# Kernel tuning notes

Hardware: AMD Instinct MI355X
Metric: run time of the kernel (lower is better)

Reference implementation:

```python
import jax, jax.numpy as jnp
import numpy as np

T, B, D, H, L = 64, 512, 1536, 1024, 4
DISCOUNT = 0.997
LAM = 0.95


def setup_inputs() -> dict:
    key = jax.random.key(0)
    ks = jax.random.split(key, 3 + L + 1)
    inp = {
        'feat': jax.random.normal(ks[0], (T, B, D), dtype=jnp.float32),
        'reward': jax.random.normal(ks[1], (T - 1, B), dtype=jnp.float32),
        'cont': jnp.ones((T, B), dtype=jnp.float32),
    }
    scale = 0.02
    dims = [D] + [H] * L
    for i in range(L):
        inp[f'W{i}'] = jax.random.normal(ks[3 + i], (dims[i], dims[i + 1]), dtype=jnp.float32) * scale
        inp[f'b{i}'] = jnp.zeros((dims[i + 1],), dtype=jnp.float32)
    inp['Wo'] = jax.random.normal(ks[3 + L], (H,), dtype=jnp.float32) * scale
    inp['bo'] = jnp.zeros((), dtype=jnp.float32)
    return inp


def reference(feat, reward, cont, W0, b0, W1, b1, W2, b2, W3, b3, Wo, bo):
    # Value-net MLP (mean of critic dist): [T, B, D] -> [T, B]
    h = feat
    for W, b in ((W0, b0), (W1, b1), (W2, b2), (W3, b3)):
        h = jax.nn.silu(h @ W + b)
    value = h @ Wo + bo  # [T, B]

    disc = cont[1:] * DISCOUNT                      # [T-1, B]
    deltas = reward + disc * value[1:] - value[:-1]  # [T-1, B]

    # GAE: adv_t = delta_t + disc_t * lambda * adv_{t+1}, adv_T = 0
    def step(adv_next, xs):
        delta, dl = xs
        adv = delta + dl * adv_next
        return adv, adv

    _, advs = jax.lax.scan(step, jnp.zeros_like(value[0]),
                           (deltas, disc * LAM), reverse=True)
    ret = advs + value[:-1]   # lambda-return target, [T-1, B]
    baseline = value[:-1]
    return ret, baseline
```

## Files before the change

kernel.cpp:

```cpp
#include <hip/hip_runtime.h>
#include <hip/hip_bf16.h>

#define T_DIM 64
#define B_DIM 512
#define D_DIM 1536
#define H_DIM 1024
#define M_DIM (T_DIM * B_DIM)
#define DISCOUNT 0.997f
#define LAM 0.95f

#define BM 256
#define BN 256
#define BK 64
#define TILES_M 128
#define TILES_N 4
#define N_XCD 8
#define GEMM_LDS_BYTES (2 * (BM + BN) * BK * 2)

typedef __bf16 bf16x8 __attribute__((ext_vector_type(8)));
typedef float  f32x4  __attribute__((ext_vector_type(4)));

__device__ __forceinline__ void async_load16(const void* g, void* l) {
    __builtin_amdgcn_global_load_lds(
        (const __attribute__((address_space(1))) void*)g,
        (__attribute__((address_space(3))) void*)l,
        16, 0, 0);
}

__device__ __forceinline__ unsigned short f2bf_raw(float f) {
    __hip_bfloat16 h = __float2bfloat16(f);
    return *reinterpret_cast<unsigned short*>(&h);
}

__global__ __launch_bounds__(256) void cvt_bf16_kernel(
    const float* __restrict__ x, __hip_bfloat16* __restrict__ y, long n4) {
    long i = (long)blockIdx.x * blockDim.x + threadIdx.x;
    if (i >= n4) return;
    float4 v = reinterpret_cast<const float4*>(x)[i];
    ushort4 o;
    o.x = f2bf_raw(v.x);
    o.y = f2bf_raw(v.y);
    o.z = f2bf_raw(v.z);
    o.w = f2bf_raw(v.w);
    reinterpret_cast<ushort4*>(y)[i] = o;
}

__global__ __launch_bounds__(256) void transpose_cvt_all_kernel(
    const float* __restrict__ W0, const float* __restrict__ W1,
    const float* __restrict__ W2, const float* __restrict__ W3,
    __hip_bfloat16* __restrict__ T0, __hip_bfloat16* __restrict__ T1,
    __hip_bfloat16* __restrict__ T2, __hip_bfloat16* __restrict__ T3) {
    __shared__ float tile[32][33];
    int z = blockIdx.z;
    const float* W;
    __hip_bfloat16* Tt;
    int K;
    if (z == 0)      { W = W0; Tt = T0; K = D_DIM; }
    else if (z == 1) { W = W1; Tt = T1; K = H_DIM; }
    else if (z == 2) { W = W2; Tt = T2; K = H_DIM; }
    else             { W = W3; Tt = T3; K = H_DIM; }
    int k0 = blockIdx.x * 32, n0 = blockIdx.y * 32;
    if (k0 >= K) return;
    int tx = threadIdx.x, ty = threadIdx.y;
    #pragma unroll
    for (int r = ty; r < 32; r += 8)
        tile[r][tx] = W[(size_t)(k0 + r) * H_DIM + n0 + tx];
    __syncthreads();
    #pragma unroll
    for (int r = ty; r < 32; r += 8)
        Tt[(size_t)(n0 + r) * K + k0 + tx] = __float2bfloat16(tile[tx][r]);
}

__global__ __launch_bounds__(512, 2) void gemm_silu_kernel(
    const __hip_bfloat16* __restrict__ A,
    const __hip_bfloat16* __restrict__ Bt,
    const float* __restrict__ bias,
    __hip_bfloat16* __restrict__ C,
    const float* __restrict__ Wo,
    float* __restrict__ value,
    int K) {

    extern __shared__ __align__(16) __hip_bfloat16 smem[];
    __hip_bfloat16* AsBuf = smem;
    __hip_bfloat16* BsBuf = smem + 2 * BM * BK;

    const int tid  = threadIdx.x;
    const int wave = tid >> 6;
    const int lane = tid & 63;
    const int sub  = lane >> 3;
    const int quad = lane >> 4;
    const int r16  = lane & 15;
    const int wm   = wave & 1;
    const int wn   = wave >> 1;

    const int l     = blockIdx.x;
    const int xcd   = l & (N_XCD - 1);
    const int local = l >> 3;
    const int tn    = local & (TILES_N - 1);
    const int tm    = (xcd << 4) | (local >> 2);
    const int m0 = tm * BM;
    const int n0 = tn * BN;

    const int scol = (((lane & 7) ^ sub) << 3);

    const __hip_bfloat16* ga[4];
    const __hip_bfloat16* gb[4];
    #pragma unroll
    for (int i = 0; i < 4; ++i) {
        int chunk = wave * 4 + i;
        ga[i] = A  + (size_t)(m0 + chunk * 8 + sub) * K + scol;
        gb[i] = Bt + (size_t)(n0 + chunk * 8 + sub) * K + scol;
    }

    f32x4 acc[8][4];
    #pragma unroll
    for (int i = 0; i < 8; ++i)
        #pragma unroll
        for (int j = 0; j < 4; ++j)
            acc[i][j] = (f32x4){0.f, 0.f, 0.f, 0.f};

    const int niter = K / BK;

    #pragma unroll
    for (int i = 0; i < 4; ++i) {
        async_load16(ga[i], &AsBuf[(wave * 4 + i) * 512]); ga[i] += BK;
        async_load16(gb[i], &BsBuf[(wave * 4 + i) * 512]); gb[i] += BK;
    }

    int p = 0;
    for (int k = 0; k < niter; ++k) {
        asm volatile("s_waitcnt vmcnt(0)" ::: "memory");
        asm volatile("s_barrier" ::: "memory");

        if (k + 1 < niter) {
            int q = p ^ 1;
            #pragma unroll
            for (int i = 0; i < 4; ++i) {
                async_load16(ga[i], &AsBuf[q * (BM * BK) + (wave * 4 + i) * 512]); ga[i] += BK;
                async_load16(gb[i], &BsBuf[q * (BM * BK) + (wave * 4 + i) * 512]); gb[i] += BK;
            }
        }

        const __hip_bfloat16* As = &AsBuf[p * (BM * BK)];
        const __hip_bfloat16* Bs = &BsBuf[p * (BM * BK)];
        #pragma unroll
        for (int kk = 0; kk < BK; kk += 32) {
            bf16x8 bf[4];
            #pragma unroll
            for (int j = 0; j < 4; ++j) {
                int n_l = wn * 64 + j * 16 + r16;
                int sb  = ((kk >> 3) + quad) ^ (n_l & 7);
                bf[j] = *reinterpret_cast<const bf16x8*>(&Bs[n_l * BK + sb * 8]);
            }
            #pragma unroll
            for (int i = 0; i < 8; ++i) {
                int m_l = wm * 128 + i * 16 + r16;
                int sa  = ((kk >> 3) + quad) ^ (m_l & 7);
                bf16x8 af = *reinterpret_cast<const bf16x8*>(&As[m_l * BK + sa * 8]);
                #pragma unroll
                for (int j = 0; j < 4; ++j)
                    acc[i][j] = __builtin_amdgcn_mfma_f32_16x16x32_bf16(
                        af, bf[j], acc[i][j], 0, 0, 0);
            }
        }
        p ^= 1;
    }

    const bool do_c = (C != nullptr);
    const bool do_v = (Wo != nullptr);
    float rowsum[8][4];
    #pragma unroll
    for (int i = 0; i < 8; ++i)
        #pragma unroll
        for (int rr = 0; rr < 4; ++rr) rowsum[i][rr] = 0.f;

    #pragma unroll
    for (int j = 0; j < 4; ++j) {
        int col = n0 + wn * 64 + j * 16 + r16;
        float bj = bias[col];
        float wj = do_v ? Wo[col] : 0.f;
        #pragma unroll
        for (int i = 0; i < 8; ++i) {
            int row_base = m0 + wm * 128 + i * 16 + quad * 4;
            #pragma unroll
            for (int rr = 0; rr < 4; ++rr) {
                float v = acc[i][j][rr] + bj;
                float s = v / (1.f + __expf(-v));
                if (do_c)
                    C[(size_t)(row_base + rr) * H_DIM + col] = __float2bfloat16(s);
                rowsum[i][rr] += s * wj;
            }
        }
    }
    if (do_v) {
        #pragma unroll
        for (int i = 0; i < 8; ++i) {
            #pragma unroll
            for (int rr = 0; rr < 4; ++rr) {
                float rs = rowsum[i][rr];
                rs += __shfl_xor(rs, 1, 64);
                rs += __shfl_xor(rs, 2, 64);
                rs += __shfl_xor(rs, 4, 64);
                rs += __shfl_xor(rs, 8, 64);
                if (r16 == 0) {
                    int row = m0 + wm * 128 + i * 16 + quad * 4 + rr;
                    atomicAdd(&value[row], rs);
                }
            }
        }
    }
}

__global__ __launch_bounds__(64) void gae_kernel(
    const float* __restrict__ value,
    const float* __restrict__ reward,
    const float* __restrict__ cont,
    const float* __restrict__ bo_p,
    float* __restrict__ out) {
    int b = blockIdx.x * blockDim.x + threadIdx.x;
    if (b >= B_DIM) return;
    float bo = bo_p[0];
    float adv = 0.f;
    float v_next = value[(T_DIM - 1) * B_DIM + b] + bo;
    for (int t = T_DIM - 2; t >= 0; --t) {
        float v_t  = value[t * B_DIM + b] + bo;
        float disc = cont[(t + 1) * B_DIM + b] * DISCOUNT;
        float delta = reward[t * B_DIM + b] + disc * v_next - v_t;
        adv = delta + disc * LAM * adv;
        out[t * B_DIM + b] = adv + v_t;
        out[(T_DIM - 1) * B_DIM + t * B_DIM + b] = v_t;
        v_next = v_t;
    }
}

extern "C" void kernel_launch(void* const* d_in, const int* in_sizes, int n_in,
                              void* d_out, int out_size, void* d_ws, size_t ws_size,
                              hipStream_t stream) {
    const float* feat   = (const float*)d_in[0];
    const float* reward = (const float*)d_in[1];
    const float* cont   = (const float*)d_in[2];
    const float* W[4]   = {(const float*)d_in[3], (const float*)d_in[5],
                           (const float*)d_in[7], (const float*)d_in[9]};
    const float* bias[4] = {(const float*)d_in[4], (const float*)d_in[6],
                            (const float*)d_in[8], (const float*)d_in[10]};
    const float* Wo = (const float*)d_in[11];
    const float* bo = (const float*)d_in[12];
    float* out = (float*)d_out;

    char* ws = (char*)d_ws;
    __hip_bfloat16* Xb = (__hip_bfloat16*)ws; ws += (size_t)M_DIM * D_DIM * 2;
    __hip_bfloat16* Ha = (__hip_bfloat16*)ws; ws += (size_t)M_DIM * H_DIM * 2;
    __hip_bfloat16* Hb = (__hip_bfloat16*)ws; ws += (size_t)M_DIM * H_DIM * 2;
    __hip_bfloat16* Wt0 = (__hip_bfloat16*)ws; ws += (size_t)H_DIM * D_DIM * 2;
    __hip_bfloat16* Wt1 = (__hip_bfloat16*)ws; ws += (size_t)H_DIM * H_DIM * 2;
    __hip_bfloat16* Wt2 = (__hip_bfloat16*)ws; ws += (size_t)H_DIM * H_DIM * 2;
    __hip_bfloat16* Wt3 = (__hip_bfloat16*)ws; ws += (size_t)H_DIM * H_DIM * 2;
    float* value = (float*)ws; ws += (size_t)M_DIM * 4;

    (void)hipFuncSetAttribute((const void*)gemm_silu_kernel,
                              hipFuncAttributeMaxDynamicSharedMemorySize,
                              GEMM_LDS_BYTES);

    long n4 = (long)M_DIM * D_DIM / 4;
    cvt_bf16_kernel<<<(int)((n4 + 255) / 256), 256, 0, stream>>>(feat, Xb, n4);

    transpose_cvt_all_kernel<<<dim3(D_DIM / 32, H_DIM / 32, 4), dim3(32, 8), 0, stream>>>(
        W[0], W[1], W[2], W[3], Wt0, Wt1, Wt2, Wt3);

    hipMemsetAsync(value, 0, (size_t)M_DIM * 4, stream);

    const int nblocks = TILES_M * TILES_N;
    gemm_silu_kernel<<<nblocks, 512, GEMM_LDS_BYTES, stream>>>(
        Xb, Wt0, bias[0], Ha, nullptr, nullptr, D_DIM);
    gemm_silu_kernel<<<nblocks, 512, GEMM_LDS_BYTES, stream>>>(
        Ha, Wt1, bias[1], Hb, nullptr, nullptr, H_DIM);
    gemm_silu_kernel<<<nblocks, 512, GEMM_LDS_BYTES, stream>>>(
        Hb, Wt2, bias[2], Ha, nullptr, nullptr, H_DIM);
    gemm_silu_kernel<<<nblocks, 512, GEMM_LDS_BYTES, stream>>>(
        Ha, Wt3, bias[3], nullptr, Wo, value, H_DIM);

    gae_kernel<<<8, 64, 0, stream>>>(value, reward, cont, bo, out);
}
```

Before: 722.5 us.

## Halve GEMM K-tile to 32 with static LDS and templated value-fusion epilogue

New measurement: 786.3 us. 8.8% more time.

```diff
diff --git a/kernel.cpp b/kernel.cpp
--- a/kernel.cpp
+++ b/kernel.cpp
@@ -11,11 +11,10 @@
 
 #define BM 256
 #define BN 256
-#define BK 64
+#define BK 32
 #define TILES_M 128
 #define TILES_N 4
 #define N_XCD 8
-#define GEMM_LDS_BYTES (2 * (BM + BN) * BK * 2)
 
 typedef __bf16 bf16x8 __attribute__((ext_vector_type(8)));
 typedef float  f32x4  __attribute__((ext_vector_type(4)));
@@ -71,7 +70,8 @@
         Tt[(size_t)(n0 + r) * K + k0 + tx] = __float2bfloat16(tile[tx][r]);
 }
 
-__global__ __launch_bounds__(512, 2) void gemm_silu_kernel(
+template <bool FUSE_VALUE>
+__global__ __launch_bounds__(512, 2) void gemm_silu_core(
     const __hip_bfloat16* __restrict__ A,
     const __hip_bfloat16* __restrict__ Bt,
     const float* __restrict__ bias,
@@ -80,14 +80,12 @@
     float* __restrict__ value,
     int K) {
 
-    extern __shared__ __align__(16) __hip_bfloat16 smem[];
-    __hip_bfloat16* AsBuf = smem;
-    __hip_bfloat16* BsBuf = smem + 2 * BM * BK;
+    __shared__ alignas(16) __hip_bfloat16 As[2][BM * BK];
+    __shared__ alignas(16) __hip_bfloat16 Bs[2][BN * BK];
 
     const int tid  = threadIdx.x;
     const int wave = tid >> 6;
     const int lane = tid & 63;
-    const int sub  = lane >> 3;
     const int quad = lane >> 4;
     const int r16  = lane & 15;
     const int wm   = wave & 1;
@@ -101,15 +99,16 @@
     const int m0 = tm * BM;
     const int n0 = tn * BN;
 
-    const int scol = (((lane & 7) ^ sub) << 3);
-
-    const __hip_bfloat16* ga[4];
-    const __hip_bfloat16* gb[4];
-    #pragma unroll
-    for (int i = 0; i < 4; ++i) {
-        int chunk = wave * 4 + i;
-        ga[i] = A  + (size_t)(m0 + chunk * 8 + sub) * K + scol;
-        gb[i] = Bt + (size_t)(n0 + chunk * 8 + sub) * K + scol;
+    const int srow  = lane >> 2;
+    const int sslot = ((lane & 3) ^ ((lane >> 3) & 3)) << 3;
+
+    const __hip_bfloat16* ga[2];
+    const __hip_bfloat16* gb[2];
+    #pragma unroll
+    for (int i = 0; i < 2; ++i) {
+        int chunk = wave * 2 + i;
+        ga[i] = A  + (size_t)(m0 + chunk * 16 + srow) * K + sslot;
+        gb[i] = Bt + (size_t)(n0 + chunk * 16 + srow) * K + sslot;
     }
 
     f32x4 acc[8][4];
@@ -122,9 +121,9 @@
     const int niter = K / BK;
 
     #pragma unroll
-    for (int i = 0; i < 4; ++i) {
-        async_load16(ga[i], &AsBuf[(wave * 4 + i) * 512]); ga[i] += BK;
-        async_load16(gb[i], &BsBuf[(wave * 4 + i) * 512]); gb[i] += BK;
+    for (int i = 0; i < 2; ++i) {
+        async_load16(ga[i], &As[0][(wave * 2 + i) * 512]); ga[i] += BK;
+        async_load16(gb[i], &Bs[0][(wave * 2 + i) * 512]); gb[i] += BK;
     }
 
     int p = 0;
@@ -135,64 +134,69 @@
         if (k + 1 < niter) {
             int q = p ^ 1;
             #pragma unroll
-            for (int i = 0; i < 4; ++i) {
-                async_load16(ga[i], &AsBuf[q * (BM * BK) + (wave * 4 + i) * 512]); ga[i] += BK;
-                async_load16(gb[i], &BsBuf[q * (BM * BK) + (wave * 4 + i) * 512]); gb[i] += BK;
-            }
-        }
-
-        const __hip_bfloat16* As = &AsBuf[p * (BM * BK)];
-        const __hip_bfloat16* Bs = &BsBuf[p * (BM * BK)];
-        #pragma unroll
-        for (int kk = 0; kk < BK; kk += 32) {
-            bf16x8 bf[4];
-            #pragma unroll
-            for (int j = 0; j < 4; ++j) {
-                int n_l = wn * 64 + j * 16 + r16;
-                int sb  = ((kk >> 3) + quad) ^ (n_l & 7);
-                bf[j] = *reinterpret_cast<const bf16x8*>(&Bs[n_l * BK + sb * 8]);
-            }
+            for (int i = 0; i < 2; ++i) {
+                async_load16(ga[i], &As[q][(wave * 2 + i) * 512]); ga[i] += BK;
+                async_load16(gb[i], &Bs[q][(wave * 2 + i) * 512]); gb[i] += BK;
+            }
+        }
+
+        bf16x8 bf[4];
+        #pragma unroll
+        for (int j = 0; j < 4; ++j) {
+            int n_l = wn * 64 + j * 16 + r16;
+            int sb  = quad ^ ((n_l >> 1) & 3);
+            bf[j] = *reinterpret_cast<const bf16x8*>(&Bs[p][n_l * BK + sb * 8]);
+        }
+        #pragma unroll
+        for (int i = 0; i < 8; ++i) {
+            int m_l = wm * 128 + i * 16 + r16;
+            int sa  = quad ^ ((m_l >> 1) & 3);
+            bf16x8 af = *reinterpret_cast<const bf16x8*>(&As[p][m_l * BK + sa * 8]);
+            #pragma unroll
+            for (int j = 0; j < 4; ++j)
+                acc[i][j] = __builtin_amdgcn_mfma_f32_16x16x32_bf16(
+                    af, bf[j], acc[i][j], 0, 0, 0);
+        }
+        p ^= 1;
+    }
+
+    if (!FUSE_VALUE) {
+        #pragma unroll
+        for (int j = 0; j < 4; ++j) {
+            int col = n0 + wn * 64 + j * 16 + r16;
+            float bj = bias[col];
             #pragma unroll
             for (int i = 0; i < 8; ++i) {
-                int m_l = wm * 128 + i * 16 + r16;
-                int sa  = ((kk >> 3) + quad) ^ (m_l & 7);
-                bf16x8 af = *reinterpret_cast<const bf16x8*>(&As[m_l * BK + sa * 8]);
+                int row_base = m0 + wm * 128 + i * 16 + quad * 4;
                 #pragma unroll
-                for (int j = 0; j < 4; ++j)
-                    acc[i][j] = __builtin_amdgcn_mfma_f32_16x16x32_bf16(
-                        af, bf[j], acc[i][j], 0, 0, 0);
-            }
-        }
-        p ^= 1;
-    }
-
-    const bool do_c = (C != nullptr);
-    const bool do_v = (Wo != nullptr);
-    float rowsum[8][4];
-    #pragma unroll
-    for (int i = 0; i < 8; ++i)
-        #pragma unroll
-        for (int rr = 0; rr < 4; ++rr) rowsum[i][rr] = 0.f;
-
-    #pragma unroll
-    for (int j = 0; j < 4; ++j) {
-        int col = n0 + wn * 64 + j * 16 + r16;
-        float bj = bias[col];
-        float wj = do_v ? Wo[col] : 0.f;
-        #pragma unroll
-        for (int i = 0; i < 8; ++i) {
-            int row_base = m0 + wm * 128 + i * 16 + quad * 4;
-            #pragma unroll
-            for (int rr = 0; rr < 4; ++rr) {
-                float v = acc[i][j][rr] + bj;
-                float s = v / (1.f + __expf(-v));
-                if (do_c)
+                for (int rr = 0; rr < 4; ++rr) {
+                    float v = acc[i][j][rr] + bj;
+                    float s = v / (1.f + __expf(-v));
                     C[(size_t)(row_base + rr) * H_DIM + col] = __float2bfloat16(s);
-                rowsum[i][rr] += s * wj;
-            }
-        }
-    }
-    if (do_v) {
+                }
+            }
+        }
+    } else {
+        float rowsum[8][4];
+        #pragma unroll
+        for (int i = 0; i < 8; ++i)
+            #pragma unroll
+            for (int rr = 0; rr < 4; ++rr) rowsum[i][rr] = 0.f;
+        #pragma unroll
+        for (int j = 0; j < 4; ++j) {
+            int col = n0 + wn * 64 + j * 16 + r16;
+            float bj = bias[col];
+            float wj = Wo[col];
+            #pragma unroll
+            for (int i = 0; i < 8; ++i) {
+                #pragma unroll
+                for (int rr = 0; rr < 4; ++rr) {
+                    float v = acc[i][j][rr] + bj;
+                    float s = v / (1.f + __expf(-v));
+                    rowsum[i][rr] += s * wj;
+                }
+            }
+        }
         #pragma unroll
         for (int i = 0; i < 8; ++i) {
             #pragma unroll
@@ -257,10 +261,6 @@
     __hip_bfloat16* Wt3 = (__hip_bfloat16*)ws; ws += (size_t)H_DIM * H_DIM * 2;
     float* value = (float*)ws; ws += (size_t)M_DIM * 4;
 
-    (void)hipFuncSetAttribute((const void*)gemm_silu_kernel,
-                              hipFuncAttributeMaxDynamicSharedMemorySize,
-                              GEMM_LDS_BYTES);
-
     long n4 = (long)M_DIM * D_DIM / 4;
     cvt_bf16_kernel<<<(int)((n4 + 255) / 256), 256, 0, stream>>>(feat, Xb, n4);
 
@@ -270,13 +270,13 @@
     hipMemsetAsync(value, 0, (size_t)M_DIM * 4, stream);
 
     const int nblocks = TILES_M * TILES_N;
-    gemm_silu_kernel<<<nblocks, 512, GEMM_LDS_BYTES, stream>>>(
+    gemm_silu_core<false><<<nblocks, 512, 0, stream>>>(
         Xb, Wt0, bias[0], Ha, nullptr, nullptr, D_DIM);
-    gemm_silu_kernel<<<nblocks, 512, GEMM_LDS_BYTES, stream>>>(
+    gemm_silu_core<false><<<nblocks, 512, 0, stream>>>(
         Ha, Wt1, bias[1], Hb, nullptr, nullptr, H_DIM);
-    gemm_silu_kernel<<<nblocks, 512, GEMM_LDS_BYTES, stream>>>(
+    gemm_silu_core<false><<<nblocks, 512, 0, stream>>>(
         Hb, Wt2, bias[2], Ha, nullptr, nullptr, H_DIM);
-    gemm_silu_kernel<<<nblocks, 512, GEMM_LDS_BYTES, stream>>>(
+    gemm_silu_core<true><<<nblocks, 512, 0, stream>>>(
         Ha, Wt3, bias[3], nullptr, Wo, value, H_DIM);
 
     gae_kernel<<<8, 64, 0, stream>>>(value, reward, cont, bo, out);
```
